# Kernel optimization log

Hardware: AMD Instinct MI355X
Metric: run time of the kernel (lower is better)

Reference implementation:

```python
import jax, jax.numpy as jnp
import numpy as np

NEG_INF = jnp.finfo(jnp.float32).min


def _continual_mask(attach_test_after, Q, K, test_num, chunk_size):
    """Boolean allowed-mask [B, 1, Q, K] replicating get_continual_mask +
    the per-batch test-query/train-key override in forward()."""
    k_train = K - test_num * chunk_size
    q_train = Q - test_num * chunk_size
    qi = jnp.arange(Q)[:, None]          # [Q,1]
    kj = jnp.arange(K)[None, :]          # [1,K]
    # base causal mask with diagonal offset K-Q (train queries)
    base = kj <= qi + (K - Q)            # [Q,K]
    # block-diagonal tril for test-query / test-key region
    dq = qi - q_train                    # local test row (negative for train rows, unused there)
    dk = kj - k_train
    block = (kj >= k_train) & (dk <= dq) & ((dk // chunk_size) == (dq // chunk_size))
    # per-batch: test query in chunk n may see train keys <= attach_test_after[b, n]
    chunk_idx = jnp.clip(dq[:, 0], 0, None) // chunk_size          # [Q]
    att = attach_test_after[:, chunk_idx]                          # [B,Q]
    train_key_allowed = kj[None, :, :] <= att[:, :, None]          # [B,Q,K]
    allowed = jnp.where(qi < q_train, base[None],
                        jnp.where(kj[None] < k_train, train_key_allowed, block[None]))
    return allowed[:, None]              # [B,1,Q,K]


def setup_inputs() -> dict:
    key = jax.random.key(0)
    k1, k2, k3, k4 = jax.random.split(key, 4)
    B, L, H, D = 4, 2048, 8, 64
    test_num, train_len = 64, 1536
    return {
        "queries": jax.random.normal(k1, (B, L, H, D), dtype=jnp.float32),
        "keys": jax.random.normal(k2, (B, L, H, D), dtype=jnp.float32),
        "values": jax.random.normal(k3, (B, L, H, D), dtype=jnp.float32),
        "attach_test_after": jax.random.randint(k4, (B, test_num), 0, train_len).astype(jnp.int64),
        "train_len": train_len,
    }


def reference(queries, keys, values, attach_test_after, train_len):
    B, Lq, H, Dqk = queries.shape
    test_num = attach_test_after.shape[1]
    chunk_size = (Lq - train_len) // test_num
    q = jnp.transpose(queries, (0, 2, 1, 3))   # [B,H,Lq,D]
    k = jnp.transpose(keys, (0, 2, 1, 3))      # [B,H,Lk,D]
    v = jnp.transpose(values, (0, 2, 1, 3))    # [B,H,Lk,Dv]
    Lk = k.shape[2]
    # vanilla path: scaled QK^T + continual mask + softmax + AV
    logits = jnp.einsum('bhmd,bhnd->bhmn', q, k) / jnp.sqrt(jnp.float32(Dqk))
    allowed = _continual_mask(attach_test_after, Lq, Lk, test_num, chunk_size)
    logits = jnp.where(allowed, logits, NEG_INF)
    attn = jax.nn.softmax(logits, axis=-1)
    out = jnp.einsum('bhmn,bhnd->bhmd', attn, v)
    return out.transpose(0, 2, 1, 3).reshape(B, Lq, H * v.shape[-1])  # b l (h d)
```

## Files before the change

### kernel.cpp

```cpp
#include <hip/hip_runtime.h>
#include <hip/hip_bf16.h>

typedef __bf16 bf16_t;
typedef __bf16 bf16x8 __attribute__((ext_vector_type(8)));
typedef float  f32x4  __attribute__((ext_vector_type(4)));

#define MFMA16(a, b, c) __builtin_amdgcn_mfma_f32_16x16x32_bf16((a), (b), (c), 0, 0, 0)

constexpr int Bc = 4, Lc = 2048, Hc = 8, Dc = 64;
constexpr int HD = Hc * Dc;
constexpr int TRAINc = 1536;
constexpr int ROWS_BLK = 64;
constexpr int KT = 64;

constexpr int PREPK_BLOCKS = (int)((size_t)Bc * Lc * Hc * Dc / 8 / 256);

__global__ void prep_fused(const float* __restrict__ K, bf16_t* __restrict__ Kb,
                           const float* __restrict__ V, bf16_t* __restrict__ Vt) {
  __shared__ bf16_t T[64][64];
  const int t = (int)threadIdx.x;

  if ((int)blockIdx.x < PREPK_BLOCKS) {
    size_t g = ((size_t)blockIdx.x * 256 + t) * 8;
    float4 a = *(const float4*)(K + g);
    float4 b = *(const float4*)(K + g + 4);
    bf16x8 v;
    v[0] = (bf16_t)a.x; v[1] = (bf16_t)a.y; v[2] = (bf16_t)a.z; v[3] = (bf16_t)a.w;
    v[4] = (bf16_t)b.x; v[5] = (bf16_t)b.y; v[6] = (bf16_t)b.z; v[7] = (bf16_t)b.w;
    *(bf16x8*)(Kb + g) = v;
    return;
  }

  const int bid = (int)blockIdx.x - PREPK_BLOCKS;
  const int kt = bid & 31, h = (bid >> 5) & 7, b = bid >> 8;
  {
    int kl = t >> 2, dp = (t & 3) << 4;
    const float* s = V + ((size_t)(b * Lc + kt * 64 + kl) * Hc + h) * Dc + dp;
    bf16x8 v0, v1;
    float4 f;
    f = *(const float4*)(s);      v0[0]=(bf16_t)f.x; v0[1]=(bf16_t)f.y; v0[2]=(bf16_t)f.z; v0[3]=(bf16_t)f.w;
    f = *(const float4*)(s + 4);  v0[4]=(bf16_t)f.x; v0[5]=(bf16_t)f.y; v0[6]=(bf16_t)f.z; v0[7]=(bf16_t)f.w;
    f = *(const float4*)(s + 8);  v1[0]=(bf16_t)f.x; v1[1]=(bf16_t)f.y; v1[2]=(bf16_t)f.z; v1[3]=(bf16_t)f.w;
    f = *(const float4*)(s + 12); v1[4]=(bf16_t)f.x; v1[5]=(bf16_t)f.y; v1[6]=(bf16_t)f.z; v1[7]=(bf16_t)f.w;
    const int x = kl >> 3;
    const int c0 = dp >> 3;
    *(bf16x8*)&T[kl][(c0 ^ x) << 3]       = v0;
    *(bf16x8*)&T[kl][((c0 + 1) ^ x) << 3] = v1;
  }
  __syncthreads();
  {
    int d = t >> 2, kp = (t & 3) << 4;
    const int xa = kp >> 3;
    const int xb = xa + 1;
    const int lo = d & 7, hi = d >> 3;
    const int x0 = ((hi ^ xa) << 3) + lo;
    const int x1 = ((hi ^ xb) << 3) + lo;
    bf16x8 o0, o1;
#pragma unroll
    for (int i = 0; i < 8; ++i) { o0[i] = T[kp + i][x0]; o1[i] = T[kp + 8 + i][x1]; }
    bf16_t* dst = Vt + ((size_t)((b * Hc + h) * Dc + d)) * Lc + kt * 64 + kp;
    *(bf16x8*)dst = o0;
    *(bf16x8*)(dst + 8) = o1;
  }
}

static __device__ __forceinline__ void load16(const bf16_t* g, bf16_t* l) {
  __builtin_amdgcn_global_load_lds(
      (const __attribute__((address_space(1))) unsigned int*)g,
      (__attribute__((address_space(3))) unsigned int*)l, 16, 0, 0);
}

__global__ __launch_bounds__(256, 4)
void continual_attn(const float* __restrict__ Qg, const bf16_t* __restrict__ Kb,
                    const bf16_t* __restrict__ Vt, const int* __restrict__ ATT,
                    float* __restrict__ OUT)
{
  __shared__ __align__(16) bf16_t Klds[2][KT * 64];
  __shared__ __align__(16) bf16_t Vlds[2][Dc * KT];
  __shared__ __align__(16) bf16_t Plds[4][16 * 64];

  const int bid  = blockIdx.x;
  const int qblk = 31 - (bid >> 5);
  const int h    = bid & 7;
  const int b    = (bid >> 3) & 3;
  const int q0   = qblk * ROWS_BLK;

  const int tid  = (int)threadIdx.x;
  const int wave = tid >> 6;
  const int lane = tid & 63;
  const int quad = lane >> 4;
  const int col  = lane & 15;
  const int qw   = q0 + wave * 16;

  const size_t bhQ = (size_t)b * Lc * HD + (size_t)h * Dc;

  const int kr = tid >> 3;
  const bf16_t* ksrcA = Kb + bhQ + (size_t)kr * HD + (((tid & 7) ^ (kr & 7)) << 3);
  const bf16_t* vsrcA = Vt + ((size_t)((b * Hc + h) * Dc + kr)) * Lc + (((tid & 7) ^ (kr & 7)) << 3);
  const bf16_t* vsrcB = vsrcA + (size_t)32 * Lc;

  bf16x8 aq[2];
  {
    const float* qp = Qg + bhQ + (size_t)(qw + col) * HD + quad * 8;
#pragma unroll
    for (int t = 0; t < 2; ++t) {
      float4 lo = *(const float4*)(qp + t * 32);
      float4 hi = *(const float4*)(qp + t * 32 + 4);
      bf16x8 v;
      v[0] = (bf16_t)(lo.x * 0.125f); v[1] = (bf16_t)(lo.y * 0.125f);
      v[2] = (bf16_t)(lo.z * 0.125f); v[3] = (bf16_t)(lo.w * 0.125f);
      v[4] = (bf16_t)(hi.x * 0.125f); v[5] = (bf16_t)(hi.y * 0.125f);
      v[6] = (bf16_t)(hi.z * 0.125f); v[7] = (bf16_t)(hi.w * 0.125f);
      aq[t] = v;
    }
  }

  const bool testblk = (q0 >= TRAINc);
  int kend[4], cstart[4], qir[4];
#pragma unroll
  for (int r = 0; r < 4; ++r) {
    int qi = qw + quad * 4 + r;
    qir[r] = qi;
    if (testblk) {
      kend[r]   = ATT[b * 64 + ((qi - TRAINc) >> 3)] + 1;
      cstart[r] = qi & ~7;
    } else {
      kend[r]   = qi + 1;
      cstart[r] = 0;
    }
  }

  int ntA, ndiag, kfull_end;
  if (testblk) {
    int c0 = (q0 - TRAINc) >> 3;
    int amax = 0, amin = 0x7fffffff;
#pragma unroll
    for (int i = 0; i < 8; ++i) {
      int a = ATT[b * 64 + c0 + i];
      amax = (a > amax) ? a : amax;
      amin = (a < amin) ? a : amin;
    }
    ntA = (amax >> 6) + 1;
    ndiag = 1;
    kfull_end = amin + 1;
  } else {
    ntA = qblk + 1;
    ndiag = 0;
    kfull_end = q0 + 1;
  }
  const int ntot = ntA + ndiag;

  float lsumL[4] = {0.f, 0.f, 0.f, 0.f};
  f32x4 o[4] = {{0,0,0,0},{0,0,0,0},{0,0,0,0},{0,0,0,0}};

  const int cA = ((quad ^ (col & 7)) << 3);
  const int c7 = col & 7;
  const int c8 = col >> 3;

  {
    bf16_t* kd = Klds[0];
    bf16_t* vd = Vlds[0];
    load16(ksrcA, kd + wave * 512);
    load16(ksrcA + (size_t)32 * HD, kd + 2048 + wave * 512);
    load16(vsrcA, vd + wave * 512);
    load16(vsrcB, vd + 2048 + wave * 512);
  }

  for (int ti = 0; ti < ntot; ++ti) {
    const int buf = ti & 1;
    __syncthreads();

    if (ti + 1 < ntot) {
      const int kn = (ti + 1 < ntA) ? (ti + 1) * KT : q0 + (ti + 1 - ntA) * KT;
      bf16_t* kd = Klds[1 - buf];
      bf16_t* vd = Vlds[1 - buf];
      load16(ksrcA + (size_t)kn * HD, kd + wave * 512);
      load16(ksrcA + (size_t)(kn + 32) * HD, kd + 2048 + wave * 512);
      load16(vsrcA + kn, vd + wave * 512);
      load16(vsrcB + kn, vd + 2048 + wave * 512);
    }

    const bf16_t* kb = Klds[buf];
    const bf16_t* vbuf = Vlds[buf];
    const int k0 = (ti < ntA) ? ti * KT : q0 + (ti - ntA) * KT;

    f32x4 sf[4] = {{0,0,0,0},{0,0,0,0},{0,0,0,0},{0,0,0,0}};
    __builtin_amdgcn_s_setprio(1);
#pragma unroll
    for (int kg = 0; kg < 4; ++kg) {
      const bf16_t* krow = kb + (kg * 16 + col) * 64;
      bf16x8 k0f = *(const bf16x8*)(krow + cA);
      bf16x8 k1f = *(const bf16x8*)(krow + (cA ^ 32));
      sf[kg] = MFMA16(aq[0], k0f, sf[kg]);
      sf[kg] = MFMA16(aq[1], k1f, sf[kg]);
    }
    __builtin_amdgcn_s_setprio(0);

    const int mode = (ti >= ntA) ? 2 : ((k0 + KT <= kfull_end) ? 0 : 1);
    if (mode == 1) {
#pragma unroll
      for (int kg = 0; kg < 4; ++kg) {
        const int kgv = k0 + kg * 16 + col;
#pragma unroll
        for (int r = 0; r < 4; ++r)
          if (kgv >= kend[r]) sf[kg][r] = -1e30f;
      }
    } else if (mode == 2) {
#pragma unroll
      for (int kg = 0; kg < 4; ++kg) {
        const int kgv = k0 + kg * 16 + col;
#pragma unroll
        for (int r = 0; r < 4; ++r)
          if (kgv < cstart[r] || kgv > qir[r]) sf[kg][r] = -1e30f;
      }
    }

    bf16_t* pw = Plds[wave];
#pragma unroll
    for (int kg = 0; kg < 4; ++kg) {
#pragma unroll
      for (int r = 0; r < 4; ++r) {
        float p = __expf(sf[kg][r]);
        lsumL[r] += p;
        const int row = quad * 4 + r;
        pw[row * 64 + (((2 * kg + c8) ^ (row & 7)) << 3) + c7] = (bf16_t)p;
      }
    }
    bf16x8 pa0 = *(const bf16x8*)&pw[col * 64 + ((quad ^ c7) << 3)];
    bf16x8 pa1 = *(const bf16x8*)&pw[col * 64 + (((4 + quad) ^ c7) << 3)];

    __builtin_amdgcn_s_setprio(1);
#pragma unroll
    for (int t = 0; t < 4; ++t) {
      const bf16_t* vrow = vbuf + (t * 16 + col) * 64;
      bf16x8 v0 = *(const bf16x8*)(vrow + cA);
      bf16x8 v1 = *(const bf16x8*)(vrow + (cA ^ 32));
      o[t] = MFMA16(pa0, v0, o[t]);
      o[t] = MFMA16(pa1, v1, o[t]);
    }
    __builtin_amdgcn_s_setprio(0);
  }

#pragma unroll
  for (int r = 0; r < 4; ++r) {
    float rs = lsumL[r];
    rs += __shfl_xor(rs, 1);
    rs += __shfl_xor(rs, 2);
    rs += __shfl_xor(rs, 4);
    rs += __shfl_xor(rs, 8);
    float inv = 1.f / rs;
    int qi = qw + quad * 4 + r;
    float* op = OUT + ((size_t)b * Lc + qi) * HD + (size_t)h * Dc + col;
    op[0]  = o[0][r] * inv;
    op[16] = o[1][r] * inv;
    op[32] = o[2][r] * inv;
    op[48] = o[3][r] * inv;
  }
}

extern "C" void kernel_launch(void* const* d_in, const int* in_sizes, int n_in,
                              void* d_out, int out_size, void* d_ws, size_t ws_size,
                              hipStream_t stream) {
  const float* Q   = (const float*)d_in[0];
  const float* K   = (const float*)d_in[1];
  const float* V   = (const float*)d_in[2];
  const int*   ATT = (const int*)d_in[3];
  float* OUT = (float*)d_out;
  (void)in_sizes; (void)n_in; (void)out_size; (void)ws_size;

  const size_t NE = (size_t)Bc * Lc * Hc * Dc;
  bf16_t* Kb = (bf16_t*)d_ws;
  bf16_t* Vt = Kb + NE;

  prep_fused<<<dim3((unsigned)(PREPK_BLOCKS + Bc * Hc * (Lc / 64))), dim3(256), 0, stream>>>(K, Kb, V, Vt);
  continual_attn<<<dim3(Bc * Hc * (Lc / ROWS_BLK)), dim3(256), 0, stream>>>(Q, Kb, Vt, ATT, OUT);
}
```

Baseline: 131.8 us.

## Double query rows per block to 128 with 8 waves sharing K/V tiles

New measurement: 133.1 us. About the same (+1.0%).

```diff
diff --git a/kernel.cpp b/kernel.cpp
--- a/kernel.cpp
+++ b/kernel.cpp
@@ -10,7 +10,7 @@
 constexpr int Bc = 4, Lc = 2048, Hc = 8, Dc = 64;
 constexpr int HD = Hc * Dc;
 constexpr int TRAINc = 1536;
-constexpr int ROWS_BLK = 64;
+constexpr int ROWS_BLK = 128;
 constexpr int KT = 64;
 
 constexpr int PREPK_BLOCKS = (int)((size_t)Bc * Lc * Hc * Dc / 8 / 256);
@@ -70,17 +70,18 @@
       (__attribute__((address_space(3))) unsigned int*)l, 16, 0, 0);
 }
 
-__global__ __launch_bounds__(256, 4)
+__global__ __launch_bounds__(512, 4)
 void continual_attn(const float* __restrict__ Qg, const bf16_t* __restrict__ Kb,
                     const bf16_t* __restrict__ Vt, const int* __restrict__ ATT,
                     float* __restrict__ OUT)
 {
   __shared__ __align__(16) bf16_t Klds[2][KT * 64];
   __shared__ __align__(16) bf16_t Vlds[2][Dc * KT];
-  __shared__ __align__(16) bf16_t Plds[4][16 * 64];
+  __shared__ __align__(16) bf16_t Plds[8][16 * 64];
 
   const int bid  = blockIdx.x;
-  const int qblk = 31 - (bid >> 5);
+  const int g    = bid >> 5;
+  const int qblk = (g < 8) ? (15 - g) : (g - 8);
   const int h    = bid & 7;
   const int b    = (bid >> 3) & 3;
   const int q0   = qblk * ROWS_BLK;
@@ -95,22 +96,23 @@
   const size_t bhQ = (size_t)b * Lc * HD + (size_t)h * Dc;
 
   const int kr = tid >> 3;
-  const bf16_t* ksrcA = Kb + bhQ + (size_t)kr * HD + (((tid & 7) ^ (kr & 7)) << 3);
-  const bf16_t* vsrcA = Vt + ((size_t)((b * Hc + h) * Dc + kr)) * Lc + (((tid & 7) ^ (kr & 7)) << 3);
-  const bf16_t* vsrcB = vsrcA + (size_t)32 * Lc;
+  const int sw = ((tid & 7) ^ (kr & 7)) << 3;
+  const bf16_t* ksrc = Kb + bhQ + (size_t)kr * HD + sw;
+  const bf16_t* vsrc = Vt + ((size_t)((b * Hc + h) * Dc + kr)) * Lc + sw;
 
   bf16x8 aq[2];
   {
     const float* qp = Qg + bhQ + (size_t)(qw + col) * HD + quad * 8;
+    const float SC = 0.125f * 1.44269504f;
 #pragma unroll
     for (int t = 0; t < 2; ++t) {
       float4 lo = *(const float4*)(qp + t * 32);
       float4 hi = *(const float4*)(qp + t * 32 + 4);
       bf16x8 v;
-      v[0] = (bf16_t)(lo.x * 0.125f); v[1] = (bf16_t)(lo.y * 0.125f);
-      v[2] = (bf16_t)(lo.z * 0.125f); v[3] = (bf16_t)(lo.w * 0.125f);
-      v[4] = (bf16_t)(hi.x * 0.125f); v[5] = (bf16_t)(hi.y * 0.125f);
-      v[6] = (bf16_t)(hi.z * 0.125f); v[7] = (bf16_t)(hi.w * 0.125f);
+      v[0] = (bf16_t)(lo.x * SC); v[1] = (bf16_t)(lo.y * SC);
+      v[2] = (bf16_t)(lo.z * SC); v[3] = (bf16_t)(lo.w * SC);
+      v[4] = (bf16_t)(hi.x * SC); v[5] = (bf16_t)(hi.y * SC);
+      v[6] = (bf16_t)(hi.z * SC); v[7] = (bf16_t)(hi.w * SC);
       aq[t] = v;
     }
   }
@@ -135,16 +137,16 @@
     int c0 = (q0 - TRAINc) >> 3;
     int amax = 0, amin = 0x7fffffff;
 #pragma unroll
-    for (int i = 0; i < 8; ++i) {
+    for (int i = 0; i < 16; ++i) {
       int a = ATT[b * 64 + c0 + i];
       amax = (a > amax) ? a : amax;
       amin = (a < amin) ? a : amin;
     }
     ntA = (amax >> 6) + 1;
-    ndiag = 1;
+    ndiag = 2;
     kfull_end = amin + 1;
   } else {
-    ntA = qblk + 1;
+    ntA = 2 * qblk + 2;
     ndiag = 0;
     kfull_end = q0 + 1;
   }
@@ -158,12 +160,8 @@
   const int c8 = col >> 3;
 
   {
-    bf16_t* kd = Klds[0];
-    bf16_t* vd = Vlds[0];
-    load16(ksrcA, kd + wave * 512);
-    load16(ksrcA + (size_t)32 * HD, kd + 2048 + wave * 512);
-    load16(vsrcA, vd + wave * 512);
-    load16(vsrcB, vd + 2048 + wave * 512);
+    load16(ksrc, Klds[0] + wave * 512);
+    load16(vsrc, Vlds[0] + wave * 512);
   }
 
   for (int ti = 0; ti < ntot; ++ti) {
@@ -172,12 +170,8 @@
 
     if (ti + 1 < ntot) {
       const int kn = (ti + 1 < ntA) ? (ti + 1) * KT : q0 + (ti + 1 - ntA) * KT;
-      bf16_t* kd = Klds[1 - buf];
-      bf16_t* vd = Vlds[1 - buf];
-      load16(ksrcA + (size_t)kn * HD, kd + wave * 512);
-      load16(ksrcA + (size_t)(kn + 32) * HD, kd + 2048 + wave * 512);
-      load16(vsrcA + kn, vd + wave * 512);
-      load16(vsrcB + kn, vd + 2048 + wave * 512);
+      load16(ksrc + (size_t)kn * HD, Klds[1 - buf] + wave * 512);
+      load16(vsrc + kn,              Vlds[1 - buf] + wave * 512);
     }
 
     const bf16_t* kb = Klds[buf];
@@ -220,7 +214,7 @@
     for (int kg = 0; kg < 4; ++kg) {
 #pragma unroll
       for (int r = 0; r < 4; ++r) {
-        float p = __expf(sf[kg][r]);
+        float p = __builtin_amdgcn_exp2f(sf[kg][r]);
         lsumL[r] += p;
         const int row = quad * 4 + r;
         pw[row * 64 + (((2 * kg + c8) ^ (row & 7)) << 3) + c7] = (bf16_t)p;
@@ -273,5 +267,5 @@
   bf16_t* Vt = Kb + NE;
 
   prep_fused<<<dim3((unsigned)(PREPK_BLOCKS + Bc * Hc * (Lc / 64))), dim3(256), 0, stream>>>(K, Kb, V, Vt);
-  continual_attn<<<dim3(Bc * Hc * (Lc / ROWS_BLK)), dim3(256), 0, stream>>>(Q, Kb, Vt, ATT, OUT);
-}
+  continual_attn<<<dim3(Bc * Hc * (Lc / ROWS_BLK)), dim3(512), 0, stream>>>(Q, Kb, Vt, ATT, OUT);
+}
```

## Compute transposed scores and keep P in registers via permlane swaps

Applied to the files above, without the earlier changes.

Measured after the change: 126.7 us. 1.04x faster.

```diff
diff --git a/kernel.cpp b/kernel.cpp
--- a/kernel.cpp
+++ b/kernel.cpp
@@ -70,6 +70,13 @@
       (__attribute__((address_space(3))) unsigned int*)l, 16, 0, 0);
 }
 
+static __device__ __forceinline__ bf16x8 mk8(unsigned w0, unsigned w1,
+                                             unsigned w2, unsigned w3) {
+  union { unsigned u[4]; bf16x8 v; } x;
+  x.u[0] = w0; x.u[1] = w1; x.u[2] = w2; x.u[3] = w3;
+  return x.v;
+}
+
 __global__ __launch_bounds__(256, 4)
 void continual_attn(const float* __restrict__ Qg, const bf16_t* __restrict__ Kb,
                     const bf16_t* __restrict__ Vt, const int* __restrict__ ATT,
@@ -77,7 +84,6 @@
 {
   __shared__ __align__(16) bf16_t Klds[2][KT * 64];
   __shared__ __align__(16) bf16_t Vlds[2][Dc * KT];
-  __shared__ __align__(16) bf16_t Plds[4][16 * 64];
 
   const int bid  = blockIdx.x;
   const int qblk = 31 - (bid >> 5);
@@ -102,32 +108,29 @@
   bf16x8 aq[2];
   {
     const float* qp = Qg + bhQ + (size_t)(qw + col) * HD + quad * 8;
+    const float SC = 0.125f * 1.44269504f;
 #pragma unroll
     for (int t = 0; t < 2; ++t) {
       float4 lo = *(const float4*)(qp + t * 32);
       float4 hi = *(const float4*)(qp + t * 32 + 4);
       bf16x8 v;
-      v[0] = (bf16_t)(lo.x * 0.125f); v[1] = (bf16_t)(lo.y * 0.125f);
-      v[2] = (bf16_t)(lo.z * 0.125f); v[3] = (bf16_t)(lo.w * 0.125f);
-      v[4] = (bf16_t)(hi.x * 0.125f); v[5] = (bf16_t)(hi.y * 0.125f);
-      v[6] = (bf16_t)(hi.z * 0.125f); v[7] = (bf16_t)(hi.w * 0.125f);
+      v[0] = (bf16_t)(lo.x * SC); v[1] = (bf16_t)(lo.y * SC);
+      v[2] = (bf16_t)(lo.z * SC); v[3] = (bf16_t)(lo.w * SC);
+      v[4] = (bf16_t)(hi.x * SC); v[5] = (bf16_t)(hi.y * SC);
+      v[6] = (bf16_t)(hi.z * SC); v[7] = (bf16_t)(hi.w * SC);
       aq[t] = v;
     }
   }
 
   const bool testblk = (q0 >= TRAINc);
-  int kend[4], cstart[4], qir[4];
-#pragma unroll
-  for (int r = 0; r < 4; ++r) {
-    int qi = qw + quad * 4 + r;
-    qir[r] = qi;
-    if (testblk) {
-      kend[r]   = ATT[b * 64 + ((qi - TRAINc) >> 3)] + 1;
-      cstart[r] = qi & ~7;
-    } else {
-      kend[r]   = qi + 1;
-      cstart[r] = 0;
-    }
+  const int qi = qw + col;
+  int kendL, cstartL;
+  if (testblk) {
+    kendL   = ATT[b * 64 + ((qi - TRAINc) >> 3)] + 1;
+    cstartL = qi & ~7;
+  } else {
+    kendL   = qi + 1;
+    cstartL = 0;
   }
 
   int ntA, ndiag, kfull_end;
@@ -150,12 +153,10 @@
   }
   const int ntot = ntA + ndiag;
 
-  float lsumL[4] = {0.f, 0.f, 0.f, 0.f};
+  float ls[4] = {0.f, 0.f, 0.f, 0.f};
   f32x4 o[4] = {{0,0,0,0},{0,0,0,0},{0,0,0,0},{0,0,0,0}};
 
   const int cA = ((quad ^ (col & 7)) << 3);
-  const int c7 = col & 7;
-  const int c8 = col >> 3;
 
   {
     bf16_t* kd = Klds[0];
@@ -191,8 +192,8 @@
       const bf16_t* krow = kb + (kg * 16 + col) * 64;
       bf16x8 k0f = *(const bf16x8*)(krow + cA);
       bf16x8 k1f = *(const bf16x8*)(krow + (cA ^ 32));
-      sf[kg] = MFMA16(aq[0], k0f, sf[kg]);
-      sf[kg] = MFMA16(aq[1], k1f, sf[kg]);
+      sf[kg] = MFMA16(k0f, aq[0], sf[kg]);
+      sf[kg] = MFMA16(k1f, aq[1], sf[kg]);
     }
     __builtin_amdgcn_s_setprio(0);
 
@@ -200,34 +201,54 @@
     if (mode == 1) {
 #pragma unroll
       for (int kg = 0; kg < 4; ++kg) {
-        const int kgv = k0 + kg * 16 + col;
+        const int kv = k0 + kg * 16 + quad * 4;
 #pragma unroll
         for (int r = 0; r < 4; ++r)
-          if (kgv >= kend[r]) sf[kg][r] = -1e30f;
+          if (kv + r >= kendL) sf[kg][r] = -1e30f;
       }
     } else if (mode == 2) {
 #pragma unroll
       for (int kg = 0; kg < 4; ++kg) {
-        const int kgv = k0 + kg * 16 + col;
+        const int kv = k0 + kg * 16 + quad * 4;
 #pragma unroll
         for (int r = 0; r < 4; ++r)
-          if (kgv < cstart[r] || kgv > qir[r]) sf[kg][r] = -1e30f;
+          if (kv + r < cstartL || kv + r > qi) sf[kg][r] = -1e30f;
       }
     }
 
-    bf16_t* pw = Plds[wave];
-#pragma unroll
-    for (int kg = 0; kg < 4; ++kg) {
+    float pvv[4][4];
+#pragma unroll
+    for (int kg = 0; kg < 4; ++kg)
 #pragma unroll
       for (int r = 0; r < 4; ++r) {
-        float p = __expf(sf[kg][r]);
-        lsumL[r] += p;
-        const int row = quad * 4 + r;
-        pw[row * 64 + (((2 * kg + c8) ^ (row & 7)) << 3) + c7] = (bf16_t)p;
+        float p = __builtin_amdgcn_exp2f(sf[kg][r]);
+        pvv[kg][r] = p;
+        ls[r] += p;
       }
-    }
-    bf16x8 pa0 = *(const bf16x8*)&pw[col * 64 + ((quad ^ c7) << 3)];
-    bf16x8 pa1 = *(const bf16x8*)&pw[col * 64 + (((4 + quad) ^ c7) << 3)];
+
+    unsigned Dw[4][2];
+#pragma unroll
+    for (int kg = 0; kg < 4; ++kg)
+#pragma unroll
+      for (int d = 0; d < 2; ++d)
+        asm("v_cvt_pk_bf16_f32 %0, %1, %2"
+            : "=v"(Dw[kg][d]) : "v"(pvv[kg][2 * d]), "v"(pvv[kg][2 * d + 1]));
+
+    unsigned a0 = Dw[0][0], b0 = Dw[1][0];
+    asm volatile("v_permlane32_swap_b32 %0, %1" : "+v"(a0), "+v"(b0));
+    asm volatile("v_permlane16_swap_b32 %0, %1" : "+v"(a0), "+v"(b0));
+    unsigned a1 = Dw[0][1], b1 = Dw[1][1];
+    asm volatile("v_permlane32_swap_b32 %0, %1" : "+v"(a1), "+v"(b1));
+    asm volatile("v_permlane16_swap_b32 %0, %1" : "+v"(a1), "+v"(b1));
+    unsigned a2 = Dw[2][0], b2 = Dw[3][0];
+    asm volatile("v_permlane32_swap_b32 %0, %1" : "+v"(a2), "+v"(b2));
+    asm volatile("v_permlane16_swap_b32 %0, %1" : "+v"(a2), "+v"(b2));
+    unsigned a3 = Dw[2][1], b3 = Dw[3][1];
+    asm volatile("v_permlane32_swap_b32 %0, %1" : "+v"(a3), "+v"(b3));
+    asm volatile("v_permlane16_swap_b32 %0, %1" : "+v"(a3), "+v"(b3));
+
+    bf16x8 pa0 = mk8(a0, a1, b0, b1);
+    bf16x8 pa1 = mk8(a2, a3, b2, b3);
 
     __builtin_amdgcn_s_setprio(1);
 #pragma unroll
@@ -241,16 +262,15 @@
     __builtin_amdgcn_s_setprio(0);
   }
 
+  float rs = (ls[0] + ls[1]) + (ls[2] + ls[3]);
+  rs += __shfl_xor(rs, 16);
+  rs += __shfl_xor(rs, 32);
 #pragma unroll
   for (int r = 0; r < 4; ++r) {
-    float rs = lsumL[r];
-    rs += __shfl_xor(rs, 1);
-    rs += __shfl_xor(rs, 2);
-    rs += __shfl_xor(rs, 4);
-    rs += __shfl_xor(rs, 8);
-    float inv = 1.f / rs;
-    int qi = qw + quad * 4 + r;
-    float* op = OUT + ((size_t)b * Lc + qi) * HD + (size_t)h * Dc + col;
+    float dr = __shfl(rs, quad * 4 + r);
+    float inv = 1.f / dr;
+    int qo = qw + quad * 4 + r;
+    float* op = OUT + ((size_t)b * Lc + qo) * HD + (size_t)h * Dc + col;
     op[0]  = o[0][r] * inv;
     op[16] = o[1][r] * inv;
     op[32] = o[2][r] * inv;
```
